# Kernel tuning notes

Measured on AMD Instinct MI355X. Metric: run time of the kernel, lower is better.

## Reference

```python
import jax, jax.numpy as jnp
import numpy as np

BIG = 1.0e6  # cost for empty groups
EPS = 1e-6

COST_ACTIVITY = 1.0
COST_GROUP = 1.0
COST_SIZE = 1.0


def setup_inputs() -> dict:
    key = jax.random.key(0)
    k1, k2, k3, k4 = jax.random.split(key, 4)
    bs, Q, C = 256, 512, 128   # batch, num_queries, num_activity_classes
    P, G = 256, 128            # num_persons, num_target_groups
    return {
        "pred_activity_logits": jax.random.normal(k1, (bs, Q, C), dtype=jnp.float32),
        "attention_logits": jax.random.normal(k2, (bs, P, Q), dtype=jnp.float32),
        "tgt_activity_ids": jax.random.randint(k3, (bs, G), 0, C),
        "tgt_group_ids": jax.random.randint(k4, (bs, P), 0, G),
    }


def reference(pred_activity_logits, attention_logits, tgt_activity_ids, tgt_group_ids):
    bs, Q, C = pred_activity_logits.shape
    P = attention_logits.shape[1]
    G = tgt_activity_ids.shape[1]

    # out_attw_b.T -> [Q, P]; log_softmax over dim 0 (queries)
    attw = jnp.transpose(attention_logits, (0, 2, 1))          # [bs, Q, P]
    logP = jax.nn.log_softmax(attw, axis=1)                    # softmax over queries
    P_qn = jnp.exp(logP)
    P_clamped = jnp.clip(P_qn, EPS, 1.0 - EPS)
    lognegP = jnp.log1p(-P_clamped)                            # [bs, Q, P]

    # one-hot grouping target: M[b, p, g] = 1 iff person p in group g
    M = jax.nn.one_hot(tgt_group_ids, G, dtype=logP.dtype)     # [bs, P, G]
    m = M.sum(axis=1)                                          # [bs, G] members per group
    nm = P - m                                                 # nonmembers per group

    # grouping cost: -mean member logP - mean nonmember log(1-P)
    mem_sum = jnp.einsum('bqp,bpg->bqg', logP, M)
    non_sum = jnp.einsum('bqp,bpg->bqg', lognegP, 1.0 - M)
    safe_m = jnp.maximum(m, 1.0)[:, None, :]
    safe_nm = jnp.maximum(nm, 1.0)[:, None, :]
    grouping_cost = -mem_sum / safe_m - non_sum / safe_nm      # [bs, Q, G]

    # size cost: |sum_p P_qn - m| / n_person
    pred_size = P_qn.sum(axis=2)                               # [bs, Q]
    size_cost = jnp.abs(pred_size[:, :, None] - m[:, None, :]) / max(float(P), 1.0)

    empty = (m == 0)[:, None, :]                               # [bs, 1, G]
    grouping_cost = jnp.where(empty, BIG, grouping_cost)
    size_cost = jnp.where(empty, BIG, size_cost)

    # activity cost: cross-entropy of query logits vs each group's activity class
    logq = jax.nn.log_softmax(pred_activity_logits, axis=-1)   # [bs, Q, C]
    idx = jnp.broadcast_to(tgt_activity_ids[:, None, :], (bs, Q, G))
    activity_cost = -jnp.take_along_axis(logq, idx, axis=2)    # [bs, Q, G]

    cost = (COST_GROUP * grouping_cost
            + COST_ACTIVITY * activity_cost
            + COST_SIZE * size_cost)
    return cost
```

## Files before the change

### kernel.cpp

```cpp
#include <hip/hip_runtime.h>

#define BS 256
#define NQ 512
#define NC 128
#define NP 256
#define NG 128
#define TQ 32
#define BIGC 1.0e6f
#define EPSC 1e-6f


__global__ __launch_bounds__(512) void pre_kernel(const float* __restrict__ att,
                                                  float* __restrict__ lse,
                                                  float* __restrict__ part) {
    __shared__ float attS[32 * NQ];
    __shared__ float invS[32];
    const int t   = threadIdx.x;
    const int blk = blockIdx.x;
    const int b   = blk >> 3;
    const int r   = t >> 4;
    const int p   = (blk & 7) * 32 + r;
    const int sub = t & 15;

    const float4* a4 = (const float4*)(att + ((size_t)(b * NP + p)) * NQ);
    float4 v[8];
#pragma unroll
    for (int i = 0; i < 8; ++i) v[i] = a4[sub + 16 * i];

    float mx = -1e30f;
#pragma unroll
    for (int i = 0; i < 8; ++i)
        mx = fmaxf(mx, fmaxf(fmaxf(v[i].x, v[i].y), fmaxf(v[i].z, v[i].w)));
#pragma unroll
    for (int off = 1; off < 16; off <<= 1) mx = fmaxf(mx, __shfl_xor(mx, off, 64));

    float s = 0.f;
#pragma unroll
    for (int i = 0; i < 8; ++i) {
        v[i].x = __expf(v[i].x - mx); v[i].y = __expf(v[i].y - mx);
        v[i].z = __expf(v[i].z - mx); v[i].w = __expf(v[i].w - mx);
        s += v[i].x + v[i].y + v[i].z + v[i].w;
        *(float4*)(attS + r * NQ + 4 * sub + 64 * i) = v[i];
    }
#pragma unroll
    for (int off = 1; off < 16; off <<= 1) s += __shfl_xor(s, off, 64);
    if (sub == 0) {
        invS[r] = 1.f / s;
        lse[b * NP + p] = mx + __logf(s);
    }
    __syncthreads();

    float sz = 0.f, sl = 0.f;
#pragma unroll 8
    for (int pp = 0; pp < 32; ++pp) {
        const float P = attS[pp * NQ + t] * invS[pp];
        sz += P;
        const float c = fminf(fmaxf(P, EPSC), 1.f - EPSC);
        sl += __logf(1.f - c);
    }
    float* basep = part + (size_t)blk * 2 * NQ;
    basep[t]      = sz;
    basep[NQ + t] = sl;
}

__global__ __launch_bounds__(512) void cost_kernel(
    const float* __restrict__ predAct,
    const float* __restrict__ att,
    const int*   __restrict__ actIds,
    const int*   __restrict__ grpIds,
    const float* __restrict__ lseAtt,
    const float* __restrict__ part,
    float*       __restrict__ out)
{
    __shared__ float xS[NP * TQ];
    __shared__ float lS[NP * TQ];
    __shared__ float lseS[NP];
    __shared__ float lseAct[TQ];
    __shared__ float szG[TQ], slG[TQ];
    __shared__ int   gidS[NP];
    __shared__ int   rankS[NP];
    __shared__ int   aidS[NG];
    __shared__ int   cntS[NG];
    __shared__ int   startS[NG];

    const int b  = blockIdx.x >> 4;
    const int q0 = (blockIdx.x & 15) * TQ;
    const int t  = threadIdx.x;

    const int pr  = t >> 3;
    const int qo4 = (t & 7) * 4;
    float4 v[4];
#pragma unroll
    for (int it = 0; it < 4; ++it)
        v[it] = *(const float4*)(att + ((size_t)(b * NP + it * 64 + pr)) * NQ + q0 + qo4);

    const int wv = t >> 6, ln = t & 63;
    float pa0[4], pa1[4];
#pragma unroll
    for (int k = 0; k < 4; ++k) {
        const float* rowp = predAct + ((size_t)(b * NQ + q0 + wv + 8 * k)) * NC;
        pa0[k] = rowp[ln]; pa1[k] = rowp[ln + 64];
    }

    if (t < NP) { lseS[t] = lseAtt[b * NP + t]; gidS[t] = grpIds[b * NP + t]; }
    if (t < NG) { aidS[t] = actIds[b * NG + t]; cntS[t] = 0; }
    if (t < 2 * TQ) {
        const int qo = t & 31, which = t >> 5;
        const float* pb = part + ((size_t)(b * 8)) * 2 * NQ + (size_t)which * NQ + q0 + qo;
        float s = 0.f;
#pragma unroll
        for (int k = 0; k < 8; ++k) s += pb[(size_t)k * 2 * NQ];
        if (which == 0) szG[qo] = s; else slG[qo] = s;
    }
    __syncthreads();

    int myPos = 0;
    if (t < NP) myPos = atomicAdd(&cntS[gidS[t]], 1);
    __syncthreads();

    if (t < 64) {
        const int c0 = cntS[2 * t], c1 = cntS[2 * t + 1];
        const int ps = c0 + c1;
        int s = ps;
#pragma unroll
        for (int off = 1; off < 64; off <<= 1) {
            const int w = __shfl_up(s, off, 64);
            if (t >= off) s += w;
        }
        startS[2 * t]     = s - ps;
        startS[2 * t + 1] = s - ps + c0;
    }
    __syncthreads();
    if (t < NP) rankS[t] = startS[gidS[t]] + myPos;
    __syncthreads();

#pragma unroll
    for (int it = 0; it < 4; ++it) {
        const int p  = it * 64 + pr;
        const float l = lseS[p];
        const int rr = rankS[p];
        float x[4], ll[4];
        const float vv[4] = {v[it].x, v[it].y, v[it].z, v[it].w};
#pragma unroll
        for (int j = 0; j < 4; ++j) {
            x[j] = vv[j] - l;
            const float e = __expf(x[j]);
            const float c = fminf(fmaxf(e, EPSC), 1.f - EPSC);
            ll[j] = __logf(1.f - c);
        }
        *(float4*)(xS + rr * TQ + qo4) = *(float4*)x;
        *(float4*)(lS + rr * TQ + qo4) = *(float4*)ll;
    }

#pragma unroll
    for (int k = 0; k < 4; ++k) {
        const int r = wv + 8 * k;
        float mx = fmaxf(pa0[k], pa1[k]);
#pragma unroll
        for (int off = 1; off < 64; off <<= 1) mx = fmaxf(mx, __shfl_xor(mx, off, 64));
        float s = __expf(pa0[k] - mx) + __expf(pa1[k] - mx);
#pragma unroll
        for (int off = 1; off < 64; off <<= 1) s += __shfl_xor(s, off, 64);
        if (ln == 0) lseAct[r] = mx + __logf(s);
    }
    __syncthreads();

    const float* actBase = predAct + ((size_t)(b * NQ + q0)) * NC;
#pragma unroll
    for (int rep = 0; rep < 2; ++rep) {
        const int idx = rep * 512 + t;
        const int qo  = idx & 31;
        const int g4  = (idx >> 5) * 4;
        const float sl = slG[qo], pz = szG[qo], la = lseAct[qo];
        float res[4];
#pragma unroll
        for (int j = 0; j < 4; ++j) {
            const int g  = g4 + j;
            const int m  = cntS[g];
            const int st = startS[g];
            float ms = 0.f, ml = 0.f;
            for (int i = 0; i < m; ++i) {
                ms += xS[(st + i) * TQ + qo];
                ml += lS[(st + i) * TQ + qo];
            }
            const float mf  = (float)m;
            const float nmf = (float)(NP - m);
            float grp = -ms / fmaxf(mf, 1.f) - (sl - ml) / fmaxf(nmf, 1.f);
            float szc = fabsf(pz - mf) * (1.f / (float)NP);
            if (m == 0) { grp = BIGC; szc = BIGC; }
            const float av = actBase[(size_t)qo * NC + aidS[g]];
            res[j] = grp + (la - av) + szc;
        }
        *(float4*)(out + ((size_t)(b * NQ + q0 + qo)) * NG + g4) = *(float4*)res;
    }
}

extern "C" void kernel_launch(void* const* d_in, const int* in_sizes, int n_in,
                              void* d_out, int out_size, void* d_ws, size_t ws_size,
                              hipStream_t stream) {
    const float* predAct = (const float*)d_in[0];
    const float* att     = (const float*)d_in[1];
    const int*   actIds  = (const int*)d_in[2];
    const int*   grpIds  = (const int*)d_in[3];
    float*       out     = (float*)d_out;
    float*       lse     = (float*)d_ws;
    float*       part    = lse + (size_t)BS * NP;

    pre_kernel<<<BS * 8, 512, 0, stream>>>(att, lse, part);
    cost_kernel<<<BS * (NQ / TQ), 512, 0, stream>>>(predAct, att, actIds, grpIds, lse, part, out);
}
```

Before: 322.1 us.

## Fold group normalization into per-person weights and gather activity logits from LDS

Each person's contribution is pre-scaled by its group's 1/m and 1/(NP-m), so the member and nonmember sums merge into one weighted sum. This halves the LDS staging buffer and the inner-loop loads. Activity logits already held in registers are written to a padded shared tile, replacing scattered global gathers. Launch bounds now ask for higher occupancy, which risks register spills.

```diff
diff --git a/kernel.cpp b/kernel.cpp
--- a/kernel.cpp
+++ b/kernel.cpp
@@ -6,6 +6,7 @@
 #define NP 256
 #define NG 128
 #define TQ 32
+#define PTS (NC + 1)
 #define BIGC 1.0e6f
 #define EPSC 1e-6f
 
@@ -63,7 +64,7 @@
     basep[NQ + t] = sl;
 }
 
-__global__ __launch_bounds__(512) void cost_kernel(
+__global__ __launch_bounds__(512, 6) void cost_kernel(
     const float* __restrict__ predAct,
     const float* __restrict__ att,
     const int*   __restrict__ actIds,
@@ -72,8 +73,8 @@
     const float* __restrict__ part,
     float*       __restrict__ out)
 {
-    __shared__ float xS[NP * TQ];
-    __shared__ float lS[NP * TQ];
+    __shared__ float wS[NP * TQ];
+    __shared__ float pTile[TQ * PTS];
     __shared__ float lseS[NP];
     __shared__ float lseAct[TQ];
     __shared__ float szG[TQ], slG[TQ];
@@ -134,22 +135,25 @@
     if (t < NP) rankS[t] = startS[gidS[t]] + myPos;
     __syncthreads();
 
-#pragma unroll
+    #pragma unroll
     for (int it = 0; it < 4; ++it) {
         const int p  = it * 64 + pr;
         const float l = lseS[p];
         const int rr = rankS[p];
-        float x[4], ll[4];
+        const int m  = cntS[gidS[p]];
+        const float im  = 1.f / (float)m;
+        const float inm = 1.f / fmaxf((float)(NP - m), 1.f);
+        float w[4];
         const float vv[4] = {v[it].x, v[it].y, v[it].z, v[it].w};
 #pragma unroll
         for (int j = 0; j < 4; ++j) {
-            x[j] = vv[j] - l;
-            const float e = __expf(x[j]);
+            const float x = vv[j] - l;
+            const float e = __expf(x);
             const float c = fminf(fmaxf(e, EPSC), 1.f - EPSC);
-            ll[j] = __logf(1.f - c);
+            const float ll = __logf(1.f - c);
+            w[j] = ll * inm - x * im;
         }
-        *(float4*)(xS + rr * TQ + qo4) = *(float4*)x;
-        *(float4*)(lS + rr * TQ + qo4) = *(float4*)ll;
+        *(float4*)(wS + rr * TQ + qo4) = *(float4*)w;
     }
 
 #pragma unroll
@@ -162,10 +166,11 @@
 #pragma unroll
         for (int off = 1; off < 64; off <<= 1) s += __shfl_xor(s, off, 64);
         if (ln == 0) lseAct[r] = mx + __logf(s);
-    }
-    __syncthreads();
-
-    const float* actBase = predAct + ((size_t)(b * NQ + q0)) * NC;
+        pTile[r * PTS + ln]      = pa0[k];
+        pTile[r * PTS + 64 + ln] = pa1[k];
+    }
+    __syncthreads();
+
 #pragma unroll
     for (int rep = 0; rep < 2; ++rep) {
         const int idx = rep * 512 + t;
@@ -178,17 +183,14 @@
             const int g  = g4 + j;
             const int m  = cntS[g];
             const int st = startS[g];
-            float ms = 0.f, ml = 0.f;
-            for (int i = 0; i < m; ++i) {
-                ms += xS[(st + i) * TQ + qo];
-                ml += lS[(st + i) * TQ + qo];
-            }
+            float s = 0.f;
+            for (int i = 0; i < m; ++i) s += wS[(st + i) * TQ + qo];
             const float mf  = (float)m;
-            const float nmf = (float)(NP - m);
-            float grp = -ms / fmaxf(mf, 1.f) - (sl - ml) / fmaxf(nmf, 1.f);
+            const float nmf = fmaxf((float)(NP - m), 1.f);
+            float grp = s - sl / nmf;
             float szc = fabsf(pz - mf) * (1.f / (float)NP);
             if (m == 0) { grp = BIGC; szc = BIGC; }
-            const float av = actBase[(size_t)qo * NC + aidS[g]];
+            const float av = pTile[qo * PTS + aidS[g]];
             res[j] = grp + (la - av) + szc;
         }
         *(float4*)(out + ((size_t)(b * NQ + q0 + qo)) * NG + g4) = *(float4*)res;
```

After: 313.7 us. 2.6% less time.
